# Kernel optimization log

Measured on AMD Instinct MI355X. Metric: run time of the kernel, lower is better.

## Reference

```python
import jax, jax.numpy as jnp
import numpy as np

B, C_IN, T, H, W = 32, 1024, 7, 14, 14
C_INTER = 512


def setup_inputs() -> dict:
    key = jax.random.key(0)
    ks = jax.random.split(key, 8)
    s = lambda fan_in: 1.0 / np.sqrt(fan_in)
    return {
        "x_window": jax.random.normal(ks[0], (B, C_IN, T, H, W), jnp.float32),
        "nodes": jax.random.normal(ks[1], (T, C_INTER), jnp.float32),
        "Wq": jax.random.normal(ks[2], (C_IN, C_INTER), jnp.float32) * s(C_IN),
        "bq": jnp.zeros((C_INTER,), jnp.float32),
        "Wk": jax.random.normal(ks[3], (C_INTER, C_INTER), jnp.float32) * s(C_INTER),
        "bk": jnp.zeros((C_INTER,), jnp.float32),
        "Wv": jax.random.normal(ks[4], (C_IN, C_INTER), jnp.float32) * s(C_IN),
        "bv": jnp.zeros((C_INTER,), jnp.float32),
        "Wo": jax.random.normal(ks[5], (C_INTER, C_IN), jnp.float32) * s(C_INTER),
        "bo": jnp.zeros((C_IN,), jnp.float32),
    }


def reference(x_window, nodes, Wq, bq, Wk, bk, Wv, bv, Wo, bo):
    # x_window: (B, C_in, T, H, W); dropout is identity at eval time.
    t_mid = x_window.shape[2] // 2
    x_item = x_window[:, :, t_mid]                                   # (B, C_in, H, W)
    # pointwise (Linear3d) projections over channel dim
    query = jnp.einsum("bchw,cd->bdhw", x_item, Wq) + bq[None, :, None, None]
    key = nodes @ Wk + bk                                            # (T, C_inter)
    value = jnp.einsum("bcthw,cd->bdthw", x_window, Wv) + bv[None, :, None, None, None]
    # per-pixel attention scores over the T node keys
    alpha = jnp.einsum("bdhw,td->bthw", query, key)                  # (B, T, H, W)
    alpha = jax.nn.softmax(alpha, axis=1)
    # per-pixel weighted temporal sum
    y = jnp.einsum("bthw,bdthw->bdhw", alpha, value)                 # (B, C_inter, H, W)
    out = jnp.einsum("bdhw,dc->bchw", y, Wo) + bo[None, :, None, None]
    return out[:, :, None]                                           # (B, C_in, 1, H, W)
```

## Files before the change

kernel.cpp:

```cpp
#include <hip/hip_runtime.h>
#include <hip/hip_bf16.h>
#include <hip/hip_cooperative_groups.h>
#include <stdint.h>

namespace cg = cooperative_groups;

#define BB    32
#define CIN   1024
#define TT    7
#define HHWW  196
#define HW4   49
#define CI    512
#define TMID  3
#define MM    (BB*HHWW)
#define NCH   16
#define CSZ   64
#define GRID  512

using bf16 = __hip_bfloat16;
typedef __attribute__((ext_vector_type(8))) short short8;
typedef __attribute__((ext_vector_type(4))) short s16x4;
typedef __attribute__((ext_vector_type(4))) float f32x4;

__device__ __forceinline__ void gload_lds16(const void* g, void* l) {
    __builtin_amdgcn_global_load_lds((const __attribute__((address_space(1))) void*)g,
                                     (__attribute__((address_space(3))) void*)l, 16, 0, 0);
}

template <int EPI>
__device__ __forceinline__ void gemm_body(const bf16* __restrict__ A, const bf16* __restrict__ Bt,
                                          void* __restrict__ Cout, const float* __restrict__ bias,
                                          int M, int N, int K, int bm, int bn,
                                          bf16* As, bf16* Bs) {
    int tid = threadIdx.x;
    int wid = tid >> 6, lane = tid & 63;
    int wr = wid >> 1, wc = wid & 1;
    f32x4 acc[4][4] = {};
    const bf16* Ab = A + (size_t)bm * 128 * K;
    const bf16* Bb = Bt + (size_t)bn * 128 * K;
    int row = lane & 15;
    int kb_base = (lane >> 4) * 8;

    for (int k0 = 0; k0 < K; k0 += 64) {
        #pragma unroll
        for (int it = 0; it < 4; ++it) {
            int e = (it * 256 + tid) * 8;
            int r = e >> 6, cc = e & 63;
            gload_lds16(Ab + (size_t)r * K + k0 + cc, &As[e]);
            gload_lds16(Bb + (size_t)r * K + k0 + cc, &Bs[e]);
        }
        __syncthreads();
        #pragma unroll
        for (int kk = 0; kk < 2; ++kk) {
            int kb = kk * 32 + kb_base;
            short8 a[4], b[4];
            #pragma unroll
            for (int mi = 0; mi < 4; ++mi) a[mi] = *(const short8*)&As[(wr * 64 + mi * 16 + row) * 64 + kb];
            #pragma unroll
            for (int ni = 0; ni < 4; ++ni) b[ni] = *(const short8*)&Bs[(wc * 64 + ni * 16 + row) * 64 + kb];
            #pragma unroll
            for (int mi = 0; mi < 4; ++mi)
                #pragma unroll
                for (int ni = 0; ni < 4; ++ni)
                    acc[mi][ni] = __builtin_amdgcn_mfma_f32_16x16x32_bf16(a[mi], b[ni], acc[mi][ni], 0, 0, 0);
        }
        __syncthreads();
    }

    int col_l = lane & 15, row_l = (lane >> 4) * 4;
    if constexpr (EPI == 0) {
        bf16* C = (bf16*)Cout;
        #pragma unroll
        for (int mi = 0; mi < 4; ++mi) {
            int row0 = bm * 128 + wr * 64 + mi * 16 + row_l;
            #pragma unroll
            for (int ni = 0; ni < 4; ++ni) {
                int col = bn * 128 + wc * 64 + ni * 16 + col_l;
                #pragma unroll
                for (int r = 0; r < 4; ++r)
                    C[(size_t)(row0 + r) * N + col] = __float2bfloat16(acc[mi][ni][r]);
            }
        }
    } else {
        float* Cf = (float*)Cout;
        #pragma unroll
        for (int ni = 0; ni < 4; ++ni) {
            int n = bn * 128 + wc * 64 + ni * 16 + col_l;
            float bz = bias[n];
            #pragma unroll
            for (int mi = 0; mi < 4; ++mi) {
                int m0 = bm * 128 + wr * 64 + mi * 16 + row_l;
                int b = m0 / HHWW;
                int hw0 = m0 - b * HHWW;
                f32x4 v = acc[mi][ni];
                v[0] += bz; v[1] += bz; v[2] += bz; v[3] += bz;
                *(f32x4*)&Cf[((size_t)b * CIN + n) * HHWW + hw0] = v;
            }
        }
    }
}

__device__ __forceinline__ void phase_prep1_unit(
    int u, int tid, float* sred,
    const float* __restrict__ nodes, const float* __restrict__ Wk, const float* __restrict__ bk,
    float* __restrict__ key,
    const float* __restrict__ Wv, const float* __restrict__ Wo,
    bf16* __restrict__ Wv_bf, bf16* __restrict__ WoT_bf,
    const float* __restrict__ bv, const float* __restrict__ bo, float* __restrict__ bvo) {
    if (u < 56) {
        int t = u >> 3, dc = u & 7;
        int d_l = tid & 63, q = tid >> 6;
        int d = dc * 64 + d_l;
        float acc = 0.f;
        const float* nr = nodes + t * CI;
        #pragma unroll 4
        for (int c = q * 128; c < q * 128 + 128; ++c)
            acc = fmaf(nr[c], Wk[(size_t)c * CI + d], acc);
        sred[q * 64 + d_l] = acc;
        __syncthreads();
        if (q == 0)
            key[t * CI + d] = sred[d_l] + sred[64 + d_l] + sred[128 + d_l] + sred[192 + d_l] + bk[d];
    } else if (u < 56 + 2048) {
        int i = (u - 56) * 256 + tid;
        Wv_bf[i] = __float2bfloat16(Wv[i]);
        int d = i >> 10, cp = i & 1023;
        WoT_bf[(size_t)cp * CI + d] = __float2bfloat16(Wo[i]);
    } else {
        int cp0 = (u - 2104) * 32;
        int cp_l = tid & 31, dq = tid >> 5;
        float acc = 0.f;
        #pragma unroll 4
        for (int d = dq * 64; d < dq * 64 + 64; ++d)
            acc = fmaf(bv[d], Wo[(size_t)d * CIN + cp0 + cp_l], acc);
        sred[dq * 32 + cp_l] = acc;
        __syncthreads();
        if (dq == 0) {
            float v = bo[cp0 + cp_l];
            #pragma unroll
            for (int g = 0; g < 8; ++g) v += sred[g * 32 + cp_l];
            bvo[cp0 + cp_l] = v;
        }
    }
}

__device__ __forceinline__ void phase_wqk_unit(
    int cbase, int tid,
    const float* __restrict__ Wq, const float* __restrict__ bq,
    const float* __restrict__ key, float* __restrict__ Wqk, float* __restrict__ bqk) {
    int c = cbase + (tid >> 6);
    int lane = tid & 63;
    if (c > CIN) return;
    const float* src = (c < CIN) ? (Wq + (size_t)c * CI) : bq;
    float acc[TT] = {};
    #pragma unroll 2
    for (int it = 0; it < CI / 64; ++it) {
        float w = src[it * 64 + lane];
        #pragma unroll
        for (int t = 0; t < TT; ++t) acc[t] = fmaf(w, key[t * CI + it * 64 + lane], acc[t]);
    }
    #pragma unroll
    for (int t = 0; t < TT; ++t) {
        float v = acc[t];
        for (int off = 32; off; off >>= 1) v += __shfl_down(v, off);
        if (lane == 0) { if (c < CIN) Wqk[c * 8 + t] = v; else bqk[t] = v; }
    }
}

__device__ __forceinline__ void phase_alpha_unit(
    int ch, int b, int tid, float* wq_s,
    const float* __restrict__ x, const float* __restrict__ Wqk, float* __restrict__ part) {
    for (int i = tid; i < CSZ * 8; i += 256) wq_s[i] = Wqk[ch * CSZ * 8 + i];
    __syncthreads();
    if (tid < HHWW) {
        float acc[TT] = {};
        const float* xb = x + (size_t)(b * CIN + ch * CSZ) * TT * HHWW + TMID * HHWW + tid;
        #pragma unroll 8
        for (int c = 0; c < CSZ; ++c) {
            float v = xb[(size_t)c * TT * HHWW];
            #pragma unroll
            for (int t = 0; t < TT; ++t) acc[t] = fmaf(v, wq_s[c * 8 + t], acc[t]);
        }
        #pragma unroll
        for (int t = 0; t < TT; ++t)
            part[((size_t)(b * NCH + ch) * TT + t) * HHWW + tid] = acc[t];
    }
}

__device__ __forceinline__ void phase_softmax_unit(
    int b, int tid,
    const float* __restrict__ part, const float* __restrict__ bqk, float* __restrict__ alphaF) {
    if (tid >= HHWW) return;
    float s[TT];
    #pragma unroll
    for (int t = 0; t < TT; ++t) s[t] = bqk[t];
    #pragma unroll
    for (int ch = 0; ch < NCH; ++ch)
        #pragma unroll
        for (int t = 0; t < TT; ++t)
            s[t] += part[((size_t)(b * NCH + ch) * TT + t) * HHWW + tid];
    float mx = s[0];
    #pragma unroll
    for (int t = 1; t < TT; ++t) mx = fmaxf(mx, s[t]);
    float e[TT], sum = 0.f;
    #pragma unroll
    for (int t = 0; t < TT; ++t) { e[t] = __expf(s[t] - mx); sum += e[t]; }
    float inv = 1.f / sum;
    #pragma unroll
    for (int t = 0; t < TT; ++t) alphaF[(size_t)b * TT * HHWW + t * HHWW + tid] = e[t] * inv;
}

__device__ __forceinline__ void phase_smxw_unit(
    int c0, int b, int tid, float* al, bf16* txp,
    const float* __restrict__ x, const float* __restrict__ alphaF, bf16* __restrict__ xw) {
    for (int i = tid; i < TT * HHWW; i += 256) al[i] = alphaF[(size_t)b * TT * HHWW + i];
    __syncthreads();
    const f32x4* xp = (const f32x4*)x;
    f32x4 acc[7] = {};
    #pragma unroll
    for (int t = 0; t < TT; ++t) {
        #pragma unroll
        for (int k = 0; k < 7; ++k) {
            int w = k * 256 + tid;
            if (k == 6 && w >= 1568) continue;
            int c_l = w / 49;
            int hw4 = w - c_l * 49;
            f32x4 a4 = *(const f32x4*)&al[t * HHWW + hw4 * 4];
            f32x4 xv = xp[((size_t)(b * CIN + c0 + c_l) * TT + t) * HW4 + hw4];
            acc[k] += a4 * xv;
        }
    }
    #pragma unroll
    for (int k = 0; k < 7; ++k) {
        int w = k * 256 + tid;
        if (k == 6 && w >= 1568) continue;
        int c_l = w / 49;
        int hw4 = w - c_l * 49;
        int v = (hw4 & 7) << 2;
        #pragma unroll
        for (int r = 0; r < 4; ++r)
            txp[(hw4 * 4 + r) * 32 + (c_l ^ v)] = __float2bfloat16(acc[k][r]);
    }
    __syncthreads();
    #pragma unroll
    for (int k = 0; k < 7; ++k) {
        int w = k * 256 + tid;
        if (k == 6 && w >= 1568) continue;
        int m = w >> 3, seg = w & 7;
        int v = ((m >> 2) & 7) << 2;
        s16x4 val = *(const s16x4*)&txp[m * 32 + ((seg * 4) ^ v)];
        *(s16x4*)&xw[(size_t)(b * HHWW + m) * CIN + c0 + seg * 4] = val;
    }
}

__global__ __launch_bounds__(256, 2) void mega(
    const float* __restrict__ x, const float* __restrict__ nodes,
    const float* __restrict__ Wq, const float* __restrict__ bq,
    const float* __restrict__ Wk, const float* __restrict__ bk,
    const float* __restrict__ Wv, const float* __restrict__ bv,
    const float* __restrict__ Wo, const float* __restrict__ bo,
    float* __restrict__ key, float* __restrict__ Wqk, float* __restrict__ bqk,
    float* __restrict__ bvo, bf16* __restrict__ Wv_bf, bf16* __restrict__ WoT_bf,
    bf16* __restrict__ WvoT, float* __restrict__ part, float* __restrict__ alphaF,
    bf16* __restrict__ xw, float* __restrict__ out) {

    cg::grid_group grid = cg::this_grid();
    __shared__ __align__(16) char smem[32768];
    bf16* As = (bf16*)smem;
    bf16* Bs = (bf16*)(smem + 16384);
    int gid = blockIdx.x, tid = threadIdx.x;

    for (int u = gid; u < 2136; u += GRID) {
        __syncthreads();
        phase_prep1_unit(u, tid, (float*)smem, nodes, Wk, bk, key, Wv, Wo, Wv_bf, WoT_bf, bv, bo, bvo);
    }
    grid.sync();

    if (gid < 64) {
        gemm_body<0>(WoT_bf, Wv_bf, (void*)WvoT, nullptr, 1024, 1024, 512, gid >> 3, gid & 7, As, Bs);
    } else if (gid < 321) {
        phase_wqk_unit((gid - 64) * 4, tid, Wq, bq, key, Wqk, bqk);
    }
    grid.sync();

    phase_alpha_unit(gid & 15, gid >> 4, tid, (float*)smem, x, Wqk, part);
    grid.sync();

    if (gid < BB) phase_softmax_unit(gid, tid, part, bqk, alphaF);
    grid.sync();

    for (int u = gid; u < 1024; u += GRID) {
        __syncthreads();
        phase_smxw_unit((u & 31) * 32, u >> 5, tid, (float*)smem, (bf16*)(smem + 5504), x, alphaF, xw);
    }
    grid.sync();

    if (gid < 392)
        gemm_body<1>(xw, WvoT, (void*)out, bvo, MM, CIN, CIN, gid >> 3, gid & 7, As, Bs);
}

__global__ __launch_bounds__(256) void k_prep1(
    const float* __restrict__ nodes, const float* __restrict__ Wk, const float* __restrict__ bk,
    float* __restrict__ key, const float* __restrict__ Wv, const float* __restrict__ Wo,
    bf16* __restrict__ Wv_bf, bf16* __restrict__ WoT_bf,
    const float* __restrict__ bv, const float* __restrict__ bo, float* __restrict__ bvo) {
    __shared__ float sred[256];
    phase_prep1_unit(blockIdx.x, threadIdx.x, sred, nodes, Wk, bk, key, Wv, Wo, Wv_bf, WoT_bf, bv, bo, bvo);
}

__global__ __launch_bounds__(256) void k_prep2(
    const bf16* __restrict__ WoT_bf, const bf16* __restrict__ Wv_bf, bf16* __restrict__ WvoT,
    const float* __restrict__ Wq, const float* __restrict__ bq,
    const float* __restrict__ key, float* __restrict__ Wqk, float* __restrict__ bqk) {
    __shared__ __align__(16) bf16 As[128 * 64];
    __shared__ __align__(16) bf16 Bs[128 * 64];
    int bid = blockIdx.x;
    if (bid < 64) gemm_body<0>(WoT_bf, Wv_bf, (void*)WvoT, nullptr, 1024, 1024, 512, bid >> 3, bid & 7, As, Bs);
    else phase_wqk_unit((bid - 64) * 4, threadIdx.x, Wq, bq, key, Wqk, bqk);
}

__global__ __launch_bounds__(256) void k_alpha(const float* __restrict__ x,
                                               const float* __restrict__ Wqk,
                                               float* __restrict__ part) {
    __shared__ float wq_s[CSZ * 8];
    phase_alpha_unit(blockIdx.x, blockIdx.y, threadIdx.x, wq_s, x, Wqk, part);
}

__global__ __launch_bounds__(256) void k_softmaxF(const float* __restrict__ part,
                                                  const float* __restrict__ bqk,
                                                  float* __restrict__ alphaF) {
    phase_softmax_unit(blockIdx.x, threadIdx.x, part, bqk, alphaF);
}

__global__ __launch_bounds__(256) void k_smxw(const float* __restrict__ x,
                                              const float* __restrict__ alphaF,
                                              bf16* __restrict__ xw) {
    __shared__ __align__(16) float al[TT * HHWW];
    __shared__ __align__(16) bf16 txp[HHWW * 32];
    phase_smxw_unit(blockIdx.x * 32, blockIdx.y, threadIdx.x, al, txp, x, alphaF, xw);
}

__global__ __launch_bounds__(256) void k_gemm1(const bf16* __restrict__ A, const bf16* __restrict__ Bt,
                                               float* __restrict__ C, const float* __restrict__ bias) {
    __shared__ __align__(16) bf16 As[128 * 64];
    __shared__ __align__(16) bf16 Bs[128 * 64];
    gemm_body<1>(A, Bt, (void*)C, bias, MM, CIN, CIN, blockIdx.x, blockIdx.y, As, Bs);
}

extern "C" void kernel_launch(void* const* d_in, const int* in_sizes, int n_in,
                              void* d_out, int out_size, void* d_ws, size_t ws_size,
                              hipStream_t stream) {
    const float* x     = (const float*)d_in[0];
    const float* nodes = (const float*)d_in[1];
    const float* Wq    = (const float*)d_in[2];
    const float* bq    = (const float*)d_in[3];
    const float* Wk    = (const float*)d_in[4];
    const float* bk    = (const float*)d_in[5];
    const float* Wv    = (const float*)d_in[6];
    const float* bv    = (const float*)d_in[7];
    const float* Wo    = (const float*)d_in[8];
    const float* bo    = (const float*)d_in[9];

    uint8_t* w = (uint8_t*)d_ws;
    size_t off = 0;
    auto alloc = [&](size_t bytes) -> void* {
        void* p = w + off;
        off = (off + bytes + 255) & ~(size_t)255;
        return p;
    };
    float* key    = (float*)alloc((size_t)TT * CI * 4);
    float* Wqk    = (float*)alloc((size_t)CIN * 8 * 4);
    float* bqk    = (float*)alloc(8 * 4);
    float* bvo    = (float*)alloc((size_t)CIN * 4);
    bf16*  Wv_bf  = (bf16*)alloc((size_t)CIN * CI * 2);
    bf16*  WoT_bf = (bf16*)alloc((size_t)CIN * CI * 2);
    bf16*  WvoT   = (bf16*)alloc((size_t)CIN * CIN * 2);
    float* part   = (float*)alloc((size_t)BB * NCH * TT * HHWW * 4);
    float* alphaF = (float*)alloc((size_t)BB * TT * HHWW * 4);
    bf16*  xw     = (bf16*)alloc((size_t)MM * CIN * 2);
    float* outp   = (float*)d_out;
    (void)ws_size;

    bool use_coop = false;
    int dev = 0;
    if (hipGetDevice(&dev) == hipSuccess) {
        int coop = 0, ncu = 0, nb = 0;
        hipDeviceGetAttribute(&coop, hipDeviceAttributeCooperativeLaunch, dev);
        hipDeviceGetAttribute(&ncu, hipDeviceAttributeMultiprocessorCount, dev);
        if (coop == 1 &&
            hipOccupancyMaxActiveBlocksPerMultiprocessor(&nb, (const void*)mega, 256, 0) == hipSuccess &&
            nb * ncu >= GRID) {
            use_coop = true;
        }
    }

    if (use_coop) {
        void* kargs[] = {
            (void*)&x, (void*)&nodes, (void*)&Wq, (void*)&bq, (void*)&Wk, (void*)&bk,
            (void*)&Wv, (void*)&bv, (void*)&Wo, (void*)&bo,
            (void*)&key, (void*)&Wqk, (void*)&bqk, (void*)&bvo,
            (void*)&Wv_bf, (void*)&WoT_bf, (void*)&WvoT, (void*)&part, (void*)&alphaF,
            (void*)&xw, (void*)&outp
        };
        if (hipLaunchCooperativeKernel((const void*)mega, dim3(GRID), dim3(256), kargs, 0, stream)
            == hipSuccess)
            return;
    }

    k_prep1<<<2136, 256, 0, stream>>>(nodes, Wk, bk, key, Wv, Wo, Wv_bf, WoT_bf, bv, bo, bvo);
    k_prep2<<<321, 256, 0, stream>>>(WoT_bf, Wv_bf, WvoT, Wq, bq, key, Wqk, bqk);
    k_alpha<<<dim3(NCH, BB), 256, 0, stream>>>(x, Wqk, part);
    k_softmaxF<<<BB, 256, 0, stream>>>(part, bqk, alphaF);
    k_smxw<<<dim3(32, BB), 256, 0, stream>>>(x, alphaF, xw);
    k_gemm1<<<dim3(49, 8), 256, 0, stream>>>(xw, WvoT, (float*)d_out, bvo);
}
```

Measured before the change: 101.3 us.

## Replace grid-wide barriers with per-batch counters and producer/consumer block split

Replaces the later grid.sync barriers in the cooperative megakernel with per-batch atomic counters. Blocks are split into a group that runs softmax and the weighted temporal sum, and a group that builds WvoT and runs the final GEMM tiles as soon as their batches are ready. The WvoT GEMM moves out of the Wqk phase so it overlaps with the alpha and weighted-sum work. The alpha partial sums are split into 32 channel chunks instead of 16 to feed two rounds over all blocks. Risks include spin-wait overhead and load imbalance between the two groups. Counters are zeroed in-kernel by block 0 before the first grid sync, so each launch resets them.

```diff
diff --git a/kernel.cpp b/kernel.cpp
--- a/kernel.cpp
+++ b/kernel.cpp
@@ -13,9 +13,10 @@
 #define CI    512
 #define TMID  3
 #define MM    (BB*HHWW)
-#define NCH   16
-#define CSZ   64
+#define NCH   32
+#define CSZ   32
 #define GRID  512
+#define NPROD 256
 
 using bf16 = __hip_bfloat16;
 typedef __attribute__((ext_vector_type(8))) short short8;
@@ -25,6 +26,14 @@
 __device__ __forceinline__ void gload_lds16(const void* g, void* l) {
     __builtin_amdgcn_global_load_lds((const __attribute__((address_space(1))) void*)g,
                                      (__attribute__((address_space(3))) void*)l, 16, 0, 0);
+}
+
+__device__ __forceinline__ void ctr_inc(int* p) {
+    __hip_atomic_fetch_add(p, 1, __ATOMIC_RELEASE, __HIP_MEMORY_SCOPE_AGENT);
+}
+__device__ __forceinline__ void ctr_wait(int* p, int tgt) {
+    while (__hip_atomic_load(p, __ATOMIC_ACQUIRE, __HIP_MEMORY_SCOPE_AGENT) < tgt)
+        __builtin_amdgcn_s_sleep(8);
 }
 
 template <int EPI>
@@ -193,7 +202,6 @@
     float s[TT];
     #pragma unroll
     for (int t = 0; t < TT; ++t) s[t] = bqk[t];
-    #pragma unroll
     for (int ch = 0; ch < NCH; ++ch)
         #pragma unroll
         for (int t = 0; t < TT; ++t)
@@ -261,7 +269,7 @@
     float* __restrict__ key, float* __restrict__ Wqk, float* __restrict__ bqk,
     float* __restrict__ bvo, bf16* __restrict__ Wv_bf, bf16* __restrict__ WoT_bf,
     bf16* __restrict__ WvoT, float* __restrict__ part, float* __restrict__ alphaF,
-    bf16* __restrict__ xw, float* __restrict__ out) {
+    bf16* __restrict__ xw, float* __restrict__ out, int* ctr) {
 
     cg::grid_group grid = cg::this_grid();
     __shared__ __align__(16) char smem[32768];
@@ -269,33 +277,65 @@
     bf16* Bs = (bf16*)(smem + 16384);
     int gid = blockIdx.x, tid = threadIdx.x;
 
+    if (gid == 0 && tid < 97) ctr[tid] = 0;
     for (int u = gid; u < 2136; u += GRID) {
         __syncthreads();
         phase_prep1_unit(u, tid, (float*)smem, nodes, Wk, bk, key, Wv, Wo, Wv_bf, WoT_bf, bv, bo, bvo);
     }
     grid.sync();
 
-    if (gid < 64) {
-        gemm_body<0>(WoT_bf, Wv_bf, (void*)WvoT, nullptr, 1024, 1024, 512, gid >> 3, gid & 7, As, Bs);
-    } else if (gid < 321) {
-        phase_wqk_unit((gid - 64) * 4, tid, Wq, bq, key, Wqk, bqk);
-    }
+    if (gid < 257) phase_wqk_unit(gid * 4, tid, Wq, bq, key, Wqk, bqk);
     grid.sync();
 
-    phase_alpha_unit(gid & 15, gid >> 4, tid, (float*)smem, x, Wqk, part);
-    grid.sync();
-
-    if (gid < BB) phase_softmax_unit(gid, tid, part, bqk, alphaF);
-    grid.sync();
-
-    for (int u = gid; u < 1024; u += GRID) {
-        __syncthreads();
-        phase_smxw_unit((u & 31) * 32, u >> 5, tid, (float*)smem, (bf16*)(smem + 5504), x, alphaF, xw);
-    }
-    grid.sync();
-
-    if (gid < 392)
-        gemm_body<1>(xw, WvoT, (void*)out, bvo, MM, CIN, CIN, gid >> 3, gid & 7, As, Bs);
+    #pragma unroll 1
+    for (int r = 0; r < 2; ++r) {
+        int u = gid + r * GRID;
+        __syncthreads();
+        phase_alpha_unit(u & (NCH - 1), u >> 5, tid, (float*)smem, x, Wqk, part);
+        __syncthreads();
+        if (tid == 0) { __threadfence(); ctr_inc(&ctr[u >> 5]); }
+    }
+
+    if (gid >= NPROD) {
+        if (gid < NPROD + 32) {
+            int b = gid - NPROD;
+            if (tid == 0) ctr_wait(&ctr[b], NCH);
+            __syncthreads();
+            phase_softmax_unit(b, tid, part, bqk, alphaF);
+            __syncthreads();
+            if (tid == 0) { __threadfence(); ctr_inc(&ctr[32 + b]); }
+        }
+        int pid = gid - NPROD;
+        #pragma unroll 1
+        for (int r = 0; r < 4; ++r) {
+            int u = pid + r * NPROD;
+            int b = u >> 5, c0 = (u & 31) * 32;
+            if (tid == 0) ctr_wait(&ctr[32 + b], 1);
+            __syncthreads();
+            phase_smxw_unit(c0, b, tid, (float*)smem, (bf16*)(smem + 5504), x, alphaF, xw);
+            __syncthreads();
+            if (tid == 0) { __threadfence(); ctr_inc(&ctr[64 + b]); }
+        }
+    } else {
+        if (gid < 64) {
+            gemm_body<0>(WoT_bf, Wv_bf, (void*)WvoT, nullptr, 1024, 1024, 512, gid >> 3, gid & 7, As, Bs);
+            __syncthreads();
+            if (tid == 0) { __threadfence(); ctr_inc(&ctr[96]); }
+        }
+        #pragma unroll 1
+        for (int t = gid; t < 392; t += NPROD) {
+            int bm = t >> 3, bn = t & 7;
+            int b0 = (bm * 128) / HHWW, b1 = (bm * 128 + 127) / HHWW;
+            if (tid == 0) {
+                ctr_wait(&ctr[64 + b0], 32);
+                ctr_wait(&ctr[64 + b1], 32);
+                ctr_wait(&ctr[96], 64);
+            }
+            __syncthreads();
+            gemm_body<1>(xw, WvoT, (void*)out, bvo, MM, CIN, CIN, bm, bn, As, Bs);
+            __syncthreads();
+        }
+    }
 }
 
 __global__ __launch_bounds__(256) void k_prep1(
@@ -377,6 +417,7 @@
     float* part   = (float*)alloc((size_t)BB * NCH * TT * HHWW * 4);
     float* alphaF = (float*)alloc((size_t)BB * TT * HHWW * 4);
     bf16*  xw     = (bf16*)alloc((size_t)MM * CIN * 2);
+    int*   ctr    = (int*)alloc(128 * 4);
     float* outp   = (float*)d_out;
     (void)ws_size;
 
@@ -399,7 +440,7 @@
             (void*)&Wv, (void*)&bv, (void*)&Wo, (void*)&bo,
             (void*)&key, (void*)&Wqk, (void*)&bqk, (void*)&bvo,
             (void*)&Wv_bf, (void*)&WoT_bf, (void*)&WvoT, (void*)&part, (void*)&alphaF,
-            (void*)&xw, (void*)&outp
+            (void*)&xw, (void*)&outp, (void*)&ctr
         };
         if (hipLaunchCooperativeKernel((const void*)mega, dim3(GRID), dim3(256), kargs, 0, stream)
             == hipSuccess)
```

Measured after the change: 103.7 us. 1.02x slower.
